# Performance work log

Hardware: AMD Instinct MI355X
Metric: run time of the kernel (lower is better)

Reference implementation:

```python
import jax, jax.numpy as jnp
import numpy as np

B, N, E = 8, 5000, 40000
F, FE, FILTERS = 64, 16, 96
LN_EPS = 1e-3  # keras LayerNormalization default epsilon


def _layer_norm(x, gamma, beta):
    mu = jnp.mean(x, axis=-1, keepdims=True)
    var = jnp.mean(jnp.square(x - mu), axis=-1, keepdims=True)
    return (x - mu) * jax.lax.rsqrt(var + LN_EPS) * gamma + beta


def setup_inputs() -> dict:
    key = jax.random.key(0)
    ks = jax.random.split(key, 8)
    nodes = jax.random.normal(ks[0], (B, N, F), dtype=jnp.float32)
    edge_features = jax.random.normal(ks[1], (B, E, FE), dtype=jnp.float32)
    edges = jax.random.randint(ks[2], (B, E, 2), 0, N, dtype=jnp.int32)
    d_msg_in = 2 * F + FE   # 144
    d_upd_in = F + FILTERS  # 160
    Wm = jax.random.normal(ks[3], (d_msg_in, FILTERS), dtype=jnp.float32) / np.sqrt(d_msg_in)
    bm = jnp.zeros((FILTERS,), dtype=jnp.float32)
    Wu = jax.random.normal(ks[4], (d_upd_in, FILTERS), dtype=jnp.float32) / np.sqrt(d_upd_in)
    bu = jnp.zeros((FILTERS,), dtype=jnp.float32)
    ln_m_gamma = jnp.ones((FILTERS,), dtype=jnp.float32)
    ln_m_beta = jnp.zeros((FILTERS,), dtype=jnp.float32)
    ln_u_gamma = jnp.ones((FILTERS,), dtype=jnp.float32)
    ln_u_beta = jnp.zeros((FILTERS,), dtype=jnp.float32)
    return {"nodes": nodes, "edge_features": edge_features, "edges": edges,
            "Wm": Wm, "bm": bm, "ln_m_gamma": ln_m_gamma, "ln_m_beta": ln_m_beta,
            "Wu": Wu, "bu": bu, "ln_u_gamma": ln_u_gamma, "ln_u_beta": ln_u_beta}


def reference(nodes, edge_features, edges, Wm, bm, ln_m_gamma, ln_m_beta,
              Wu, bu, ln_u_gamma, ln_u_beta):
    b, n, f = nodes.shape
    e = edges.shape[1]
    # gather endpoint features: (B,E,2,F) -> (B,E,2F)   [tf.gather batch_dims=1 + reshape]
    gathered = jax.vmap(lambda nd, ed: nd[ed])(nodes, edges)
    messages_in = gathered.reshape(b, e, 2 * f)
    msg_in = jnp.concatenate([messages_in, edge_features], axis=-1)
    # message layer: Dense -> relu -> LayerNorm
    messages = jax.nn.relu(jnp.einsum('bec,cd->bed', msg_in, Wm) + bm)
    messages = _layer_norm(messages, ln_m_gamma, ln_m_beta)
    # aggregate: per-batch unsorted_segment_sum over destination node edges[...,1]
    aggregated = jax.vmap(
        lambda m, dst: jax.ops.segment_sum(m, dst, num_segments=n)
    )(messages, edges[..., 1])
    # update layer on [nodes, aggregated]: Dense -> relu -> LayerNorm
    upd_in = jnp.concatenate([nodes, aggregated], axis=-1)
    updated = jax.nn.relu(jnp.einsum('bnc,cd->bnd', upd_in, Wu) + bu)
    updated_nodes = _layer_norm(updated, ln_u_gamma, ln_u_beta)
    return updated_nodes, messages
```

## Files before the change

### kernel.cpp

```cpp
#include <hip/hip_runtime.h>
#include <hip/hip_bf16.h>

typedef short s16x8 __attribute__((ext_vector_type(8)));
typedef float f32x4 __attribute__((ext_vector_type(4)));

namespace {
constexpr int kB   = 8;
constexpr int kN   = 5000;
constexpr int kE   = 40000;
constexpr int kF   = 64;
constexpr int kFE  = 16;
constexpr int kFil = 96;
constexpr float kEps = 1e-3f;
constexpr int kBN = kB * kN;
constexpr int kBE = kB * kE;
constexpr int kKp = 160;
constexpr int kLd = 168;
constexpr int kBM = 128;
}

__device__ inline unsigned short f2bf(float x) {
    unsigned u = __float_as_uint(x);
    u += 0x7FFFu + ((u >> 16) & 1u);
    return (unsigned short)(u >> 16);
}

__device__ inline s16x8 pack8(const float4& a, const float4& b) {
    union { s16x8 s; __hip_bfloat162 h[4]; } r;
    r.h[0] = __float22bfloat162_rn(make_float2(a.x, a.y));
    r.h[1] = __float22bfloat162_rn(make_float2(a.z, a.w));
    r.h[2] = __float22bfloat162_rn(make_float2(b.x, b.y));
    r.h[3] = __float22bfloat162_rn(make_float2(b.z, b.w));
    return r.s;
}

__global__ void prep_wT(const float* __restrict__ Wm, const float* __restrict__ Wu,
                        short* __restrict__ wmT, short* __restrict__ wuT) {
    const int t = blockIdx.x * 256 + threadIdx.x;
    if (t >= 96 * kKp) return;
    const int n = t / kKp, k = t % kKp;
    wmT[t] = (k < 144) ? (short)f2bf(Wm[(size_t)k * 96 + n]) : (short)0;
    wuT[t] = (short)f2bf(Wu[(size_t)k * 96 + n]);
}

__device__ inline void gemm_ln_store(const short* sX, const short* sB,
                                     const float* __restrict__ bias,
                                     const float* __restrict__ gamma_,
                                     const float* __restrict__ beta_,
                                     float* __restrict__ out,
                                     const int* __restrict__ edges2,
                                     float* __restrict__ aggOut,
                                     int rowBase, int rowMax) {
    const int tid  = threadIdx.x;
    const int w    = tid >> 6;
    const int lane = tid & 63;
    const int cl   = lane & 15;
    const int quad = lane >> 4;

    f32x4 acc[6] = {};
    const short* aBase = sX + (16 * w + cl) * kLd + quad * 8;
#pragma unroll
    for (int ks = 0; ks < 5; ++ks) {
        s16x8 a = *reinterpret_cast<const s16x8*>(aBase + ks * 32);
#pragma unroll
        for (int t = 0; t < 6; ++t) {
            s16x8 b = *reinterpret_cast<const s16x8*>(
                sB + (16 * t + cl) * kLd + ks * 32 + quad * 8);
            acc[t] = __builtin_amdgcn_mfma_f32_16x16x32_bf16(a, b, acc[t], 0, 0, 0);
        }
    }

    float bmv[6], gv[6], bv[6];
#pragma unroll
    for (int t = 0; t < 6; ++t) {
        const int c = 16 * t + cl;
        bmv[t] = bias[c]; gv[t] = gamma_[c]; bv[t] = beta_[c];
    }
#pragma unroll
    for (int j = 0; j < 4; ++j) {
        float v0[6];
        float s = 0.f;
#pragma unroll
        for (int t = 0; t < 6; ++t) {
            v0[t] = fmaxf(acc[t][j] + bmv[t], 0.f);
            s += v0[t];
        }
        s += __shfl_xor(s, 1); s += __shfl_xor(s, 2);
        s += __shfl_xor(s, 4); s += __shfl_xor(s, 8);
        const float mu = s * (1.f / 96.f);
        float q = 0.f;
#pragma unroll
        for (int t = 0; t < 6; ++t) {
            const float d = v0[t] - mu;
            q = fmaf(d, d, q);
        }
        q += __shfl_xor(q, 1); q += __shfl_xor(q, 2);
        q += __shfl_xor(q, 4); q += __shfl_xor(q, 8);
        const float inv = rsqrtf(q * (1.f / 96.f) + kEps);
        const int row = rowBase + 16 * w + 4 * quad + j;
        if (row < rowMax) {
            float ov[6];
#pragma unroll
            for (int t = 0; t < 6; ++t)
                ov[t] = (v0[t] - mu) * inv * gv[t] + bv[t];
            float* orow = out + (size_t)row * kFil;
#pragma unroll
            for (int t = 0; t < 6; ++t)
                orow[16 * t + cl] = ov[t];
            if (aggOut) {
                const int b  = row / kE;
                const int dn = edges2[(size_t)row * 2 + 1];
                float* arow = aggOut + ((size_t)b * kN + dn) * kFil;
#pragma unroll
                for (int t = 0; t < 6; ++t)
                    unsafeAtomicAdd(&arow[16 * t + cl], ov[t]);
            }
        }
    }
}

__global__ __launch_bounds__(512) void msg_mfma(
    const float* __restrict__ nodes, const float* __restrict__ efeat,
    const int* __restrict__ edges, const short* __restrict__ wmT,
    const float* __restrict__ bm, const float* __restrict__ g,
    const float* __restrict__ be, float* __restrict__ out_msg,
    float* __restrict__ agg) {
    __shared__ short sX[kBM * kLd];
    __shared__ short sB[96 * kLd];
    const int tid = threadIdx.x;
    if (tid < 256) {
        const int r = tid >> 1, half = tid & 1;
        const int edge = blockIdx.x * kBM + r;
        const int b = edge / kE;
        short* dstRow = sX + r * kLd;
        if (half == 0) {
            const int s = edges[(size_t)edge * 2];
            const float4* p = reinterpret_cast<const float4*>(
                nodes + ((size_t)b * kN + s) * kF);
#pragma unroll
            for (int c = 0; c < 8; ++c)
                *reinterpret_cast<s16x8*>(dstRow + 8 * c) = pack8(p[2 * c], p[2 * c + 1]);
        } else {
            const int d = edges[(size_t)edge * 2 + 1];
            const float4* p = reinterpret_cast<const float4*>(
                nodes + ((size_t)b * kN + d) * kF);
#pragma unroll
            for (int c = 0; c < 8; ++c)
                *reinterpret_cast<s16x8*>(dstRow + 64 + 8 * c) = pack8(p[2 * c], p[2 * c + 1]);
            const float4* pe = reinterpret_cast<const float4*>(efeat + (size_t)edge * kFE);
#pragma unroll
            for (int c = 0; c < 2; ++c)
                *reinterpret_cast<s16x8*>(dstRow + 128 + 8 * c) = pack8(pe[2 * c], pe[2 * c + 1]);
            s16x8 z = {};
            *reinterpret_cast<s16x8*>(dstRow + 144) = z;
            *reinterpret_cast<s16x8*>(dstRow + 152) = z;
        }
    } else {
        for (int i = tid - 256; i < 96 * kKp / 8; i += 256) {
            const int n = i / 20, c = i % 20;
            *reinterpret_cast<s16x8*>(sB + n * kLd + 8 * c) =
                *reinterpret_cast<const s16x8*>(wmT + n * kKp + 8 * c);
        }
    }
    __syncthreads();
    gemm_ln_store(sX, sB, bm, g, be, out_msg, edges, agg,
                  blockIdx.x * kBM, kBE);
}

__global__ __launch_bounds__(512) void upd_mfma(
    const float* __restrict__ nodes, const float* __restrict__ agg,
    const short* __restrict__ wuT, const float* __restrict__ bu,
    const float* __restrict__ g, const float* __restrict__ be,
    float* __restrict__ out_upd) {
    __shared__ short sX[kBM * kLd];
    __shared__ short sB[96 * kLd];
    const int tid = threadIdx.x;
    if (tid < 256) {
        const int r = tid >> 1, half = tid & 1;
        const int node = blockIdx.x * kBM + r;
        const bool ok = node < kBN;
        short* dstRow = sX + r * kLd;
        const s16x8 z = {};
        if (half == 0) {
            const float4* p = reinterpret_cast<const float4*>(
                nodes + (size_t)(ok ? node : 0) * kF);
#pragma unroll
            for (int c = 0; c < 8; ++c)
                *reinterpret_cast<s16x8*>(dstRow + 8 * c) =
                    ok ? pack8(p[2 * c], p[2 * c + 1]) : z;
        } else {
            const float4* p = reinterpret_cast<const float4*>(
                agg + (size_t)(ok ? node : 0) * kFil);
#pragma unroll
            for (int c = 0; c < 12; ++c)
                *reinterpret_cast<s16x8*>(dstRow + 64 + 8 * c) =
                    ok ? pack8(p[2 * c], p[2 * c + 1]) : z;
        }
    } else {
        for (int i = tid - 256; i < 96 * kKp / 8; i += 256) {
            const int n = i / 20, c = i % 20;
            *reinterpret_cast<s16x8*>(sB + n * kLd + 8 * c) =
                *reinterpret_cast<const s16x8*>(wuT + n * kKp + 8 * c);
        }
    }
    __syncthreads();
    gemm_ln_store(sX, sB, bu, g, be, out_upd, nullptr, nullptr,
                  blockIdx.x * kBM, kBN);
}

extern "C" void kernel_launch(void* const* d_in, const int* in_sizes, int n_in,
                              void* d_out, int out_size, void* d_ws, size_t ws_size,
                              hipStream_t stream) {
    const float* nodes  = (const float*)d_in[0];
    const float* efeat  = (const float*)d_in[1];
    const int*   edges  = (const int*)d_in[2];
    const float* Wm     = (const float*)d_in[3];
    const float* bm     = (const float*)d_in[4];
    const float* ln_m_g = (const float*)d_in[5];
    const float* ln_m_b = (const float*)d_in[6];
    const float* Wu     = (const float*)d_in[7];
    const float* bu     = (const float*)d_in[8];
    const float* ln_u_g = (const float*)d_in[9];
    const float* ln_u_b = (const float*)d_in[10];

    float* out_upd = (float*)d_out;
    float* out_msg = (float*)d_out + (size_t)kBN * kFil;

    short* wmT = (short*)d_ws;
    short* wuT = wmT + 96 * kKp;
    float* agg = (float*)(wuT + 96 * kKp);

    hipMemsetAsync(agg, 0, (size_t)kBN * kFil * sizeof(float), stream);
    prep_wT<<<(96 * kKp + 255) / 256, 256, 0, stream>>>(Wm, Wu, wmT, wuT);

    msg_mfma<<<kBE / kBM, 512, 0, stream>>>(
        nodes, efeat, edges, wmT, bm, ln_m_g, ln_m_b, out_msg, agg);
    upd_mfma<<<(kBN + kBM - 1) / kBM, 512, 0, stream>>>(
        nodes, agg, wuT, bu, ln_u_g, ln_u_b, out_upd);
}
```

Measured before the change: 290.5 us.

## Load MFMA A-fragments directly from global into registers, dropping LDS staging

The message and update kernels no longer stage the gathered input rows into a shared-memory tile. Each lane now loads its own bf16 A-fragment (8 floats per k-step) straight from global memory into registers, following the MFMA operand layout. All 512 threads share the weight-tile copy, and launch bounds now request 4 blocks per CU. This removes LDS writes and reads plus their footprint for more occupancy, at the cost of less coalesced 32-byte global accesses per lane.

```diff
diff --git a/kernel.cpp b/kernel.cpp
--- a/kernel.cpp
+++ b/kernel.cpp
@@ -34,6 +34,11 @@
     return r.s;
 }
 
+__device__ inline s16x8 loadA8(const float* __restrict__ p) {
+    const float4* q = reinterpret_cast<const float4*>(p);
+    return pack8(q[0], q[1]);
+}
+
 __global__ void prep_wT(const float* __restrict__ Wm, const float* __restrict__ Wu,
                         short* __restrict__ wmT, short* __restrict__ wuT) {
     const int t = blockIdx.x * 256 + threadIdx.x;
@@ -43,7 +48,7 @@
     wuT[t] = (short)f2bf(Wu[(size_t)k * 96 + n]);
 }
 
-__device__ inline void gemm_ln_store(const short* sX, const short* sB,
+__device__ inline void gemm_ln_store(const s16x8 a[5], const short* sB,
                                      const float* __restrict__ bias,
                                      const float* __restrict__ gamma_,
                                      const float* __restrict__ beta_,
@@ -58,15 +63,13 @@
     const int quad = lane >> 4;
 
     f32x4 acc[6] = {};
-    const short* aBase = sX + (16 * w + cl) * kLd + quad * 8;
 #pragma unroll
     for (int ks = 0; ks < 5; ++ks) {
-        s16x8 a = *reinterpret_cast<const s16x8*>(aBase + ks * 32);
 #pragma unroll
         for (int t = 0; t < 6; ++t) {
             s16x8 b = *reinterpret_cast<const s16x8*>(
                 sB + (16 * t + cl) * kLd + ks * 32 + quad * 8);
-            acc[t] = __builtin_amdgcn_mfma_f32_16x16x32_bf16(a, b, acc[t], 0, 0, 0);
+            acc[t] = __builtin_amdgcn_mfma_f32_16x16x32_bf16(a[ks], b, acc[t], 0, 0, 0);
         }
     }
 
@@ -108,103 +111,89 @@
             for (int t = 0; t < 6; ++t)
                 orow[16 * t + cl] = ov[t];
             if (aggOut) {
-                const int b  = row / kE;
+                const int ob = row / kE;
                 const int dn = edges2[(size_t)row * 2 + 1];
-                float* arow = aggOut + ((size_t)b * kN + dn) * kFil;
+                float* arow = aggOut + ((size_t)ob * kN + dn) * kFil;
 #pragma unroll
                 for (int t = 0; t < 6; ++t)
-                    unsafeAtomicAdd(&arow[16 * t + cl], ov[t]);
+                    unsafeAtomicAdd(arow + 16 * t + cl, ov[t]);
             }
         }
     }
 }
 
-__global__ __launch_bounds__(512) void msg_mfma(
+__global__ __launch_bounds__(512, 4) void msg_mfma(
     const float* __restrict__ nodes, const float* __restrict__ efeat,
     const int* __restrict__ edges, const short* __restrict__ wmT,
     const float* __restrict__ bm, const float* __restrict__ g,
     const float* __restrict__ be, float* __restrict__ out_msg,
     float* __restrict__ agg) {
-    __shared__ short sX[kBM * kLd];
     __shared__ short sB[96 * kLd];
-    const int tid = threadIdx.x;
-    if (tid < 256) {
-        const int r = tid >> 1, half = tid & 1;
-        const int edge = blockIdx.x * kBM + r;
-        const int b = edge / kE;
-        short* dstRow = sX + r * kLd;
-        if (half == 0) {
-            const int s = edges[(size_t)edge * 2];
-            const float4* p = reinterpret_cast<const float4*>(
-                nodes + ((size_t)b * kN + s) * kF);
-#pragma unroll
-            for (int c = 0; c < 8; ++c)
-                *reinterpret_cast<s16x8*>(dstRow + 8 * c) = pack8(p[2 * c], p[2 * c + 1]);
-        } else {
-            const int d = edges[(size_t)edge * 2 + 1];
-            const float4* p = reinterpret_cast<const float4*>(
-                nodes + ((size_t)b * kN + d) * kF);
-#pragma unroll
-            for (int c = 0; c < 8; ++c)
-                *reinterpret_cast<s16x8*>(dstRow + 64 + 8 * c) = pack8(p[2 * c], p[2 * c + 1]);
-            const float4* pe = reinterpret_cast<const float4*>(efeat + (size_t)edge * kFE);
-#pragma unroll
-            for (int c = 0; c < 2; ++c)
-                *reinterpret_cast<s16x8*>(dstRow + 128 + 8 * c) = pack8(pe[2 * c], pe[2 * c + 1]);
-            s16x8 z = {};
-            *reinterpret_cast<s16x8*>(dstRow + 144) = z;
-            *reinterpret_cast<s16x8*>(dstRow + 152) = z;
-        }
+    const int tid  = threadIdx.x;
+    const int w    = tid >> 6;
+    const int lane = tid & 63;
+    const int cl   = lane & 15;
+    const int quad = lane >> 4;
+
+    const int row = blockIdx.x * kBM + 16 * w + cl;
+    const int b   = row / kE;
+    const int2 e2 = reinterpret_cast<const int2*>(edges)[row];
+    const float* srcp = nodes + ((size_t)b * kN + e2.x) * kF + 8 * quad;
+    const float* dstp = nodes + ((size_t)b * kN + e2.y) * kF + 8 * quad;
+
+    s16x8 a[5];
+    a[0] = loadA8(srcp);
+    a[1] = loadA8(srcp + 32);
+    a[2] = loadA8(dstp);
+    a[3] = loadA8(dstp + 32);
+    if (quad < 2) {
+        a[4] = loadA8(efeat + (size_t)row * kFE + 8 * quad);
     } else {
-        for (int i = tid - 256; i < 96 * kKp / 8; i += 256) {
-            const int n = i / 20, c = i % 20;
-            *reinterpret_cast<s16x8*>(sB + n * kLd + 8 * c) =
-                *reinterpret_cast<const s16x8*>(wmT + n * kKp + 8 * c);
-        }
+        s16x8 z = {};
+        a[4] = z;
+    }
+
+    for (int i = tid; i < 96 * kKp / 8; i += 512) {
+        const int n = i / 20, c = i % 20;
+        *reinterpret_cast<s16x8*>(sB + n * kLd + 8 * c) =
+            *reinterpret_cast<const s16x8*>(wmT + n * kKp + 8 * c);
     }
     __syncthreads();
-    gemm_ln_store(sX, sB, bm, g, be, out_msg, edges, agg,
+    gemm_ln_store(a, sB, bm, g, be, out_msg, edges, agg,
                   blockIdx.x * kBM, kBE);
 }
 
-__global__ __launch_bounds__(512) void upd_mfma(
+__global__ __launch_bounds__(512, 4) void upd_mfma(
     const float* __restrict__ nodes, const float* __restrict__ agg,
     const short* __restrict__ wuT, const float* __restrict__ bu,
     const float* __restrict__ g, const float* __restrict__ be,
     float* __restrict__ out_upd) {
-    __shared__ short sX[kBM * kLd];
     __shared__ short sB[96 * kLd];
-    const int tid = threadIdx.x;
-    if (tid < 256) {
-        const int r = tid >> 1, half = tid & 1;
-        const int node = blockIdx.x * kBM + r;
-        const bool ok = node < kBN;
-        short* dstRow = sX + r * kLd;
-        const s16x8 z = {};
-        if (half == 0) {
-            const float4* p = reinterpret_cast<const float4*>(
-                nodes + (size_t)(ok ? node : 0) * kF);
-#pragma unroll
-            for (int c = 0; c < 8; ++c)
-                *reinterpret_cast<s16x8*>(dstRow + 8 * c) =
-                    ok ? pack8(p[2 * c], p[2 * c + 1]) : z;
-        } else {
-            const float4* p = reinterpret_cast<const float4*>(
-                agg + (size_t)(ok ? node : 0) * kFil);
-#pragma unroll
-            for (int c = 0; c < 12; ++c)
-                *reinterpret_cast<s16x8*>(dstRow + 64 + 8 * c) =
-                    ok ? pack8(p[2 * c], p[2 * c + 1]) : z;
-        }
-    } else {
-        for (int i = tid - 256; i < 96 * kKp / 8; i += 256) {
-            const int n = i / 20, c = i % 20;
-            *reinterpret_cast<s16x8*>(sB + n * kLd + 8 * c) =
-                *reinterpret_cast<const s16x8*>(wuT + n * kKp + 8 * c);
-        }
+    const int tid  = threadIdx.x;
+    const int w    = tid >> 6;
+    const int lane = tid & 63;
+    const int cl   = lane & 15;
+    const int quad = lane >> 4;
+
+    const int node0 = blockIdx.x * kBM + 16 * w + cl;
+    const int node  = (node0 < kBN) ? node0 : (kBN - 1);
+    const float* np = nodes + (size_t)node * kF + 8 * quad;
+    const float* ap = agg + (size_t)node * kFil;
+
+    s16x8 a[5];
+    a[0] = loadA8(np);
+    a[1] = loadA8(np + 32);
+    a[2] = loadA8(ap + 8 * quad);
+    a[3] = loadA8(ap + 32 + 8 * quad);
+    a[4] = loadA8(ap + 64 + 8 * quad);
+
+    for (int i = tid; i < 96 * kKp / 8; i += 512) {
+        const int n = i / 20, c = i % 20;
+        *reinterpret_cast<s16x8*>(sB + n * kLd + 8 * c) =
+            *reinterpret_cast<const s16x8*>(wuT + n * kKp + 8 * c);
     }
     __syncthreads();
-    gemm_ln_store(sX, sB, bu, g, be, out_upd, nullptr, nullptr,
+    gemm_ln_store(a, sB, bu, g, be, out_upd, nullptr, nullptr,
                   blockIdx.x * kBM, kBN);
 }
 
```

After: 292.7 us. About the same (+0.7%).
